# Kernel tuning notes

Hardware: AMD Instinct MI355X
Metric: run time of the kernel (lower is better)

Reference implementation:

```python
import jax, jax.numpy as jnp
import numpy as np

DIM = 256
NUM_HEADS = 8
RATIO = 4
K_SAMPLES = 2
B, C, H, W = 2, 256, 64, 64


def setup_inputs() -> dict:
    key = jax.random.key(0)
    ks = jax.random.split(key, 12)
    N_low = (H // RATIO) * (W // RATIO)
    s = 0.02
    return {
        "q_high_feat": jax.random.normal(ks[0], (B, C, H, W), dtype=jnp.float32),
        "k_high_feat": jax.random.normal(ks[1], (B, C, H, W), dtype=jnp.float32),
        "v_high_feat": jax.random.normal(ks[2], (B, C, H, W), dtype=jnp.float32),
        "coarse_attn_map": jax.random.uniform(ks[3], (B, N_low, N_low), dtype=jnp.float32),
        "Wq": jax.random.normal(ks[4], (C, C), dtype=jnp.float32) * s,
        "bq": jnp.zeros((C,), dtype=jnp.float32),
        "Wk": jax.random.normal(ks[5], (C, C), dtype=jnp.float32) * s,
        "bk": jnp.zeros((C,), dtype=jnp.float32),
        "Wv": jax.random.normal(ks[6], (C, C), dtype=jnp.float32) * s,
        "bv": jnp.zeros((C,), dtype=jnp.float32),
        "Wo": jax.random.normal(ks[7], (C, C), dtype=jnp.float32) * s,
        "bo": jnp.zeros((C,), dtype=jnp.float32),
    }


def _sparse_indices(coarse_attn_map, H, W):
    # top-k coarse blocks per low-res query, expanded to high-res key indices
    H_low, W_low = H // RATIO, W // RATIO
    Bm, N_low, _ = coarse_attn_map.shape
    _, topk = jax.lax.top_k(coarse_attn_map, K_SAMPLES)          # (B, N_low, k)
    r0 = (topk // W_low) * RATIO                                  # top-left row
    c0 = (topk % W_low) * RATIO                                   # top-left col
    dr, dc = jnp.meshgrid(jnp.arange(RATIO), jnp.arange(RATIO), indexing='ij')
    dr, dc = dr.reshape(-1), dc.reshape(-1)                       # (ratio^2,)
    rows = r0[..., None] + dr                                     # (B, N_low, k, r2)
    cols = c0[..., None] + dc
    idx1d = (rows * W + cols).reshape(Bm, N_low, -1)              # (B, N_low, k*r2)
    # each low-res query row is repeated ratio^2 times (as in the torch code)
    return jnp.repeat(idx1d, RATIO * RATIO, axis=1)               # (B, N_high, K)


def reference(q_high_feat, k_high_feat, v_high_feat, coarse_attn_map,
              Wq, bq, Wk, bk, Wv, bv, Wo, bo):
    Bm, Cm, Hm, Wm = q_high_feat.shape
    N = Hm * Wm
    hd = Cm // NUM_HEADS
    scale = hd ** -0.5

    q_seq = q_high_feat.reshape(Bm, Cm, N).transpose(0, 2, 1)     # (B, N, C)
    k_seq = k_high_feat.reshape(Bm, Cm, N).transpose(0, 2, 1)
    v_seq = v_high_feat.reshape(Bm, Cm, N).transpose(0, 2, 1)

    final_idx = _sparse_indices(coarse_attn_map, Hm, Wm)          # (B, N, K)
    K_len = final_idx.shape[-1]

    q_proj = q_seq @ Wq + bq
    k_proj = k_seq @ Wk + bk
    v_proj = v_seq @ Wv + bv

    gather = jax.vmap(lambda p, i: p[i])                          # per-batch gather
    k_sp = gather(k_proj, final_idx)                              # (B, N, K, C)
    v_sp = gather(v_proj, final_idx)

    q = q_proj.reshape(Bm, N, NUM_HEADS, hd).transpose(0, 2, 1, 3)            # (B,h,N,d)
    k = k_sp.reshape(Bm, N, K_len, NUM_HEADS, hd).transpose(0, 3, 1, 2, 4)    # (B,h,N,K,d)
    v = v_sp.reshape(Bm, N, K_len, NUM_HEADS, hd).transpose(0, 3, 1, 2, 4)

    attn = jnp.einsum('bhnd,bhnkd->bhnk', q, k) * scale
    attn = jax.nn.softmax(attn, axis=-1)
    x = jnp.einsum('bhnk,bhnkd->bhnd', attn, v)
    x = x.transpose(0, 2, 1, 3).reshape(Bm, N, Cm)
    out = x @ Wo + bo
    return out.transpose(0, 2, 1).reshape(Bm, Cm, Hm, Wm)
```

## Files before the change

kernel.cpp:

```cpp
#include <hip/hip_runtime.h>
#include <hip/hip_bf16.h>
#include <cstddef>

#define BB 2
#define CC 256
#define HH 64
#define WW 64
#define NN 4096
#define NH 8
#define HD 32
#define NLOW 256
#define KLEN 32

typedef __attribute__((ext_vector_type(8))) short short8;
typedef __attribute__((ext_vector_type(4))) float float4v;

__device__ __forceinline__ float b2f(short s) {
    union { unsigned u; float f; } x;
    x.u = ((unsigned)(unsigned short)s) << 16;
    return x.f;
}
__device__ __forceinline__ short f2b(float f) {
    __hip_bfloat16 h = __float2bfloat16(f);
    return __builtin_bit_cast(short, h);
}

__global__ __launch_bounds__(256) void topk_kernel(const float* __restrict__ coarse,
                                                   int* __restrict__ fidx) {
    const int w = threadIdx.x >> 6, l = threadIdx.x & 63;
    const int row = blockIdx.x * 4 + w;
    const float* r = coarse + (size_t)row * NLOW;
    float4v x = *(const float4v*)&r[l * 4];
    const int base = l * 4;
    float v1 = x[0]; int i1 = base;
    float v2 = x[1]; int i2 = base + 1;
    if (v2 > v1) { float tv = v1; v1 = v2; v2 = tv; int ti = i1; i1 = i2; i2 = ti; }
    #pragma unroll
    for (int j = 2; j < 4; ++j) {
        float e = x[j]; int ei = base + j;
        if (e > v1)      { v2 = v1; i2 = i1; v1 = e; i1 = ei; }
        else if (e > v2) { v2 = e;  i2 = ei; }
    }
    #pragma unroll
    for (int off = 1; off < 64; off <<= 1) {
        float ov1 = __shfl_xor(v1, off), ov2 = __shfl_xor(v2, off);
        int   oi1 = __shfl_xor(i1, off), oi2 = __shfl_xor(i2, off);
        bool aw = (v1 > ov1) || (v1 == ov1 && i1 < oi1);
        float nv1 = aw ? v1 : ov1;  int ni1 = aw ? i1 : oi1;
        float c1v = aw ? ov1 : v1;  int c1i = aw ? oi1 : i1;
        float c2v = aw ? v2 : ov2;  int c2i = aw ? i2 : oi2;
        bool bw = (c1v > c2v) || (c1v == c2v && c1i < c2i);
        v1 = nv1; i1 = ni1;
        v2 = bw ? c1v : c2v; i2 = bw ? c1i : c2i;
    }
    if (l < 32) {
        int s = l >> 4, jj = l & 15;
        int idx = s ? i2 : i1;
        int rr = jj >> 2, cc2 = jj & 3;
        fidx[(size_t)row * KLEN + l] =
            ((idx >> 4) * 4 + rr) * WW + (idx & 15) * 4 + cc2;
    }
}

__device__ __forceinline__ void trans_tile(const float* __restrict__ src, size_t soff,
                                           int sld, short* __restrict__ dst,
                                           size_t doff, int dld) {
    __shared__ float tile[64 * 65];
    const int t = threadIdx.x;
    #pragma unroll
    for (int p = 0; p < 4; ++p) {
        int r  = p * 16 + (t >> 4);
        int c4 = (t & 15) * 4;
        float4v v = *(const float4v*)&src[soff + (size_t)r * sld + c4];
        tile[r * 65 + c4 + 0] = v[0];
        tile[r * 65 + c4 + 1] = v[1];
        tile[r * 65 + c4 + 2] = v[2];
        tile[r * 65 + c4 + 3] = v[3];
    }
    __syncthreads();
    #pragma unroll
    for (int p = 0; p < 2; ++p) {
        int n  = p * 32 + (t >> 3);
        int c0 = (t & 7) * 8;
        short8 o;
        #pragma unroll
        for (int j = 0; j < 8; ++j) o[j] = f2b(tile[(c0 + j) * 65 + n]);
        *(short8*)&dst[doff + (size_t)n * dld + c0] = o;
    }
}

__global__ __launch_bounds__(256) void transpose_feat(
    const float* __restrict__ q, const float* __restrict__ k,
    const float* __restrict__ v, short* __restrict__ qt,
    short* __restrict__ kt, short* __restrict__ vt) {
    const int z = blockIdx.z;
    const float* src = (z < 2) ? q : (z < 4) ? k : v;
    short* dst       = (z < 2) ? qt : (z < 4) ? kt : vt;
    const int b = z & 1;
    const int n0 = blockIdx.x * 64, c0 = blockIdx.y * 64;
    trans_tile(src, (size_t)b * CC * NN + (size_t)c0 * NN + n0, NN,
               dst, ((size_t)b * NN + n0) * CC + c0, CC);
}

__global__ __launch_bounds__(256) void transpose_w(
    const float* __restrict__ Wq, const float* __restrict__ Wk,
    const float* __restrict__ Wv, const float* __restrict__ Wo,
    short* __restrict__ Wt) {
    const int z = blockIdx.z;
    const float* src = (z == 0) ? Wq : (z == 1) ? Wk : (z == 2) ? Wv : Wo;
    short* dst = Wt + (size_t)z * CC * CC;
    const int co0 = blockIdx.x * 64, ci0 = blockIdx.y * 64;
    trans_tile(src, (size_t)ci0 * CC + co0, CC,
               dst, (size_t)co0 * CC + ci0, CC);
}

__device__ __forceinline__ void gemm_core_64x64(
    const short* __restrict__ A, int am0, const short* __restrict__ Bt, int bn0,
    short* As, short* Bs, float4v acc[4]) {
    const int t = threadIdx.x;
    const int w = t >> 6, lane = t & 63;
    const int l16 = lane & 15, quad = lane >> 4;
    for (int k0 = 0; k0 < CC; k0 += 64) {
        __syncthreads();
        #pragma unroll
        for (int g = 0; g < 2; ++g) {
            int p = (w * 2 + g) * 64 + lane;
            int m = p >> 3;
            int cl8 = (((p & 7) ^ (m & 7)) << 3);
            short8 av = *(const short8*)(A  + (size_t)(am0 + m) * CC + k0 + cl8);
            short8 bv = *(const short8*)(Bt + (size_t)(bn0 + m) * CC + k0 + cl8);
            *(short8*)((char*)As + (size_t)p * 16) = av;
            *(short8*)((char*)Bs + (size_t)p * 16) = bv;
        }
        __syncthreads();
        #pragma unroll
        for (int s = 0; s < 2; ++s) {
            const int Ra = 16 * w + l16;
            short8 af = *(const short8*)((const char*)As + Ra * 128 +
                                         (((s * 4 + quad) ^ (Ra & 7)) << 4));
            #pragma unroll
            for (int nt = 0; nt < 4; ++nt) {
                const int Rb = nt * 16 + l16;
                short8 bf = *(const short8*)((const char*)Bs + Rb * 128 +
                                             (((s * 4 + quad) ^ (Rb & 7)) << 4));
                acc[nt] = __builtin_amdgcn_mfma_f32_16x16x32_bf16(af, bf, acc[nt], 0, 0, 0);
            }
        }
    }
}

__global__ __launch_bounds__(256) void proj_gemm(
    const short* __restrict__ qt, const short* __restrict__ kt,
    const short* __restrict__ vt, const short* __restrict__ Wt,
    const float* __restrict__ bq, const float* __restrict__ bk,
    const float* __restrict__ bv,
    short* __restrict__ qp, short* __restrict__ kp, short* __restrict__ vp) {
    const int which = blockIdx.z;
    const short* A  = which == 0 ? qt : which == 1 ? kt : vt;
    const short* B  = Wt + (size_t)which * CC * CC;
    const float* bias = which == 0 ? bq : which == 1 ? bk : bv;
    short* outp     = which == 0 ? qp : which == 1 ? kp : vp;
    const int am0 = blockIdx.x * 64;
    const int nt0 = blockIdx.y * 64;

    __shared__ short As[64 * 64];
    __shared__ short Bs[64 * 64];
    float4v acc[4];
    #pragma unroll
    for (int i = 0; i < 4; ++i) acc[i] = (float4v)(0.f);

    gemm_core_64x64(A, am0, B, nt0, As, Bs, acc);

    const int t = threadIdx.x;
    const int w = t >> 6, lane = t & 63;
    const int l16 = lane & 15, quad = lane >> 4;
    #pragma unroll
    for (int nt = 0; nt < 4; ++nt) {
        int col = nt0 + nt * 16 + l16;
        float bv_ = bias[col];
        #pragma unroll
        for (int r = 0; r < 4; ++r) {
            int m = am0 + 16 * w + quad * 4 + r;
            outp[(size_t)m * CC + col] = f2b(acc[nt][r] + bv_);
        }
    }
}

#define KSTR 264

__global__ __launch_bounds__(256) void attn_kernel(
    const short* __restrict__ qp, const short* __restrict__ kp,
    const short* __restrict__ vp, const int* __restrict__ fidx,
    short* __restrict__ xo) {
    const int low = blockIdx.x, b = blockIdx.y;
    const int t = threadIdx.x;

    __shared__ short Ks[32 * KSTR];
    __shared__ short Vs[32 * KSTR];
    __shared__ int idx_s[KLEN];

    if (t < KLEN) {
        int idx = fidx[(size_t)(b * NLOW + low) * KLEN + t];
        idx_s[t] = idx < 0 ? 0 : (idx > NN - 1 ? NN - 1 : idx);
    }
    __syncthreads();

    const int* kpi = (const int*)kp;
    const int* vpi = (const int*)vp;
    const int half = t >> 7, col = t & 127;
    for (int j = 0; j < KLEN; j += 2) {
        int key = j + half;
        size_t base = (size_t)(b * NN + idx_s[key]) * (CC / 2);
        ((int*)&Ks[key * KSTR])[col] = kpi[base + col];
        ((int*)&Vs[key * KSTR])[col] = vpi[base + col];
    }
    __syncthreads();

    const int qi = t >> 4, h = (t >> 1) & 7, dh = t & 1;
    const int n = low * 16 + qi;
    const short* qrow = qp + (size_t)(b * NN + n) * CC + h * HD;

    float qv[HD];
    #pragma unroll
    for (int c = 0; c < 4; ++c) {
        short8 v = *(const short8*)&qrow[c * 8];
        #pragma unroll
        for (int e = 0; e < 8; ++e) qv[c * 8 + e] = b2f(v[e]);
    }

    const float scale = 0.17677669529663687f;
    float sc[KLEN];
    float mx = -1e30f;
    for (int j = 0; j < KLEN; ++j) {
        const short* kr = &Ks[j * KSTR + h * HD];
        float s = 0.f;
        #pragma unroll
        for (int c = 0; c < 4; ++c) {
            short8 v = *(const short8*)&kr[c * 8];
            #pragma unroll
            for (int e = 0; e < 8; ++e) s += qv[c * 8 + e] * b2f(v[e]);
        }
        s *= scale;
        sc[j] = s;
        mx = fmaxf(mx, s);
    }
    float denom = 0.f;
    #pragma unroll
    for (int j = 0; j < KLEN; ++j) { sc[j] = __expf(sc[j] - mx); denom += sc[j]; }
    const float inv = 1.f / denom;

    float ov[16];
    #pragma unroll
    for (int d = 0; d < 16; ++d) ov[d] = 0.f;
    for (int j = 0; j < KLEN; ++j) {
        float p = sc[j] * inv;
        const short* vr = &Vs[j * KSTR + h * HD + dh * 16];
        #pragma unroll
        for (int c = 0; c < 2; ++c) {
            short8 v = *(const short8*)&vr[c * 8];
            #pragma unroll
            for (int e = 0; e < 8; ++e) ov[c * 8 + e] += p * b2f(v[e]);
        }
    }

    short* xrow = xo + (size_t)(b * NN + n) * CC + h * HD + dh * 16;
    #pragma unroll
    for (int c = 0; c < 2; ++c) {
        short8 v;
        #pragma unroll
        for (int e = 0; e < 8; ++e) v[e] = f2b(ov[c * 8 + e]);
        *(short8*)&xrow[c * 8] = v;
    }
}

__global__ __launch_bounds__(256) void outproj_gemm(
    const short* __restrict__ x, const short* __restrict__ Wto,
    const float* __restrict__ bo, float* __restrict__ out) {
    const int mt  = blockIdx.x;
    const int am0 = mt * 64;
    const int nt0 = blockIdx.y * 64;
    const int b   = mt >> 6;
    const int n0  = (mt & 63) * 64;

    __shared__ short As[64 * 64];
    __shared__ short Bs[64 * 64];
    __shared__ float Cs[64 * 65];

    float4v acc[4];
    #pragma unroll
    for (int i = 0; i < 4; ++i) acc[i] = (float4v)(0.f);

    gemm_core_64x64(x, am0, Wto, nt0, As, Bs, acc);

    const int t = threadIdx.x;
    const int w = t >> 6, lane = t & 63;
    const int l16 = lane & 15, quad = lane >> 4;
    __syncthreads();
    #pragma unroll
    for (int nt = 0; nt < 4; ++nt) {
        float bias = bo[nt0 + nt * 16 + l16];
        #pragma unroll
        for (int r = 0; r < 4; ++r) {
            int m = 16 * w + quad * 4 + r;
            Cs[m * 65 + nt * 16 + l16] = acc[nt][r] + bias;
        }
    }
    __syncthreads();
    #pragma unroll
    for (int p = 0; p < 16; ++p) {
        int cl = (t >> 6) + 4 * p;
        int nl = t & 63;
        out[(size_t)(b * CC + nt0 + cl) * NN + n0 + nl] = Cs[nl * 65 + cl];
    }
}

extern "C" void kernel_launch(void* const* d_in, const int* in_sizes, int n_in,
                              void* d_out, int out_size, void* d_ws, size_t ws_size,
                              hipStream_t stream) {
    const float* q      = (const float*)d_in[0];
    const float* k      = (const float*)d_in[1];
    const float* v      = (const float*)d_in[2];
    const float* coarse = (const float*)d_in[3];
    const float* Wq     = (const float*)d_in[4];
    const float* bq     = (const float*)d_in[5];
    const float* Wk     = (const float*)d_in[6];
    const float* bk     = (const float*)d_in[7];
    const float* Wv     = (const float*)d_in[8];
    const float* bv     = (const float*)d_in[9];
    const float* Wo     = (const float*)d_in[10];
    const float* bo     = (const float*)d_in[11];

    char* ws = (char*)d_ws;
    const size_t MB4 = (size_t)BB * NN * CC * 2;
    short* qt = (short*)(ws);
    short* kt = (short*)(ws + MB4);
    short* vt = (short*)(ws + 2 * MB4);
    short* qp = (short*)(ws + 3 * MB4);
    short* kp = (short*)(ws + 4 * MB4);
    short* vp = (short*)(ws + 5 * MB4);
    short* Wt = (short*)(ws + 6 * MB4);
    int* fidx = (int*)(ws + 6 * MB4 + 4 * (size_t)CC * CC * 2);
    short* xo = qt;

    topk_kernel<<<128, 256, 0, stream>>>(coarse, fidx);
    transpose_feat<<<dim3(64, 4, 6), 256, 0, stream>>>(q, k, v, qt, kt, vt);
    transpose_w<<<dim3(4, 4, 4), 256, 0, stream>>>(Wq, Wk, Wv, Wo, Wt);
    proj_gemm<<<dim3(128, 4, 3), 256, 0, stream>>>(qt, kt, vt, Wt, bq, bk, bv,
                                                   qp, kp, vp);
    attn_kernel<<<dim3(NLOW, BB), 256, 0, stream>>>(qp, kp, vp, fidx, xo);
    outproj_gemm<<<dim3(128, 4), 256, 0, stream>>>(xo, Wt + 3 * CC * CC, bo,
                                                   (float*)d_out);
}
```

Baseline: 129.9 us.

## Merge prep kernels, enlarge projection GEMM M-tile, split attention dot across lane pair

Folds topk, feature transpose and weight transpose into one prep_kernel launch, removing two kernel launches. The projection GEMM now computes 128-row tiles per block so each loaded B fragment is reused across two M sub-tiles, halving the grid. The attention kernel has each thread of a pair load only half of q and k and combine partial dot products with a shuffle, which cuts register use and duplicated loads. The cost is more registers per GEMM thread and fewer blocks in the projection grid.

```diff
diff --git a/kernel.cpp b/kernel.cpp
--- a/kernel.cpp
+++ b/kernel.cpp
@@ -25,10 +25,63 @@
     return __builtin_bit_cast(short, h);
 }
 
-__global__ __launch_bounds__(256) void topk_kernel(const float* __restrict__ coarse,
-                                                   int* __restrict__ fidx) {
+__device__ __forceinline__ void trans_tile(const float* __restrict__ src, size_t soff,
+                                           int sld, short* __restrict__ dst,
+                                           size_t doff, int dld) {
+    __shared__ float tile[64 * 65];
+    const int t = threadIdx.x;
+    #pragma unroll
+    for (int p = 0; p < 4; ++p) {
+        int r  = p * 16 + (t >> 4);
+        int c4 = (t & 15) * 4;
+        float4v v = *(const float4v*)&src[soff + (size_t)r * sld + c4];
+        tile[r * 65 + c4 + 0] = v[0];
+        tile[r * 65 + c4 + 1] = v[1];
+        tile[r * 65 + c4 + 2] = v[2];
+        tile[r * 65 + c4 + 3] = v[3];
+    }
+    __syncthreads();
+    #pragma unroll
+    for (int p = 0; p < 2; ++p) {
+        int n  = p * 32 + (t >> 3);
+        int c0 = (t & 7) * 8;
+        short8 o;
+        #pragma unroll
+        for (int j = 0; j < 8; ++j) o[j] = f2b(tile[(c0 + j) * 65 + n]);
+        *(short8*)&dst[doff + (size_t)n * dld + c0] = o;
+    }
+}
+
+__global__ __launch_bounds__(256) void prep_kernel(
+    const float* __restrict__ q, const float* __restrict__ k,
+    const float* __restrict__ v, const float* __restrict__ Wq,
+    const float* __restrict__ Wk, const float* __restrict__ Wv,
+    const float* __restrict__ Wo, const float* __restrict__ coarse,
+    short* __restrict__ qt, short* __restrict__ kt, short* __restrict__ vt,
+    short* __restrict__ Wt, int* __restrict__ fidx) {
+    const int z = blockIdx.z;
+    if (z < 6) {
+        const float* src = (z < 2) ? q : (z < 4) ? k : v;
+        short* dst       = (z < 2) ? qt : (z < 4) ? kt : vt;
+        const int b = z & 1;
+        const int n0 = blockIdx.x * 64, c0 = blockIdx.y * 64;
+        trans_tile(src, (size_t)b * CC * NN + (size_t)c0 * NN + n0, NN,
+                   dst, ((size_t)b * NN + n0) * CC + c0, CC);
+        return;
+    }
+    const int id = blockIdx.y * 64 + blockIdx.x;
+    if (id < 64) {
+        const int wz = id >> 4, tile = id & 15;
+        const float* src = (wz == 0) ? Wq : (wz == 1) ? Wk : (wz == 2) ? Wv : Wo;
+        short* dst = Wt + (size_t)wz * CC * CC;
+        const int co0 = (tile >> 2) * 64, ci0 = (tile & 3) * 64;
+        trans_tile(src, (size_t)ci0 * CC + co0, CC,
+                   dst, (size_t)co0 * CC + ci0, CC);
+        return;
+    }
+    if (id >= 192) return;
     const int w = threadIdx.x >> 6, l = threadIdx.x & 63;
-    const int row = blockIdx.x * 4 + w;
+    const int row = (id - 64) * 4 + w;
     const float* r = coarse + (size_t)row * NLOW;
     float4v x = *(const float4v*)&r[l * 4];
     const int base = l * 4;
@@ -62,88 +115,50 @@
     }
 }
 
-__device__ __forceinline__ void trans_tile(const float* __restrict__ src, size_t soff,
-                                           int sld, short* __restrict__ dst,
-                                           size_t doff, int dld) {
-    __shared__ float tile[64 * 65];
-    const int t = threadIdx.x;
-    #pragma unroll
-    for (int p = 0; p < 4; ++p) {
-        int r  = p * 16 + (t >> 4);
-        int c4 = (t & 15) * 4;
-        float4v v = *(const float4v*)&src[soff + (size_t)r * sld + c4];
-        tile[r * 65 + c4 + 0] = v[0];
-        tile[r * 65 + c4 + 1] = v[1];
-        tile[r * 65 + c4 + 2] = v[2];
-        tile[r * 65 + c4 + 3] = v[3];
-    }
-    __syncthreads();
-    #pragma unroll
-    for (int p = 0; p < 2; ++p) {
-        int n  = p * 32 + (t >> 3);
-        int c0 = (t & 7) * 8;
-        short8 o;
-        #pragma unroll
-        for (int j = 0; j < 8; ++j) o[j] = f2b(tile[(c0 + j) * 65 + n]);
-        *(short8*)&dst[doff + (size_t)n * dld + c0] = o;
-    }
-}
-
-__global__ __launch_bounds__(256) void transpose_feat(
-    const float* __restrict__ q, const float* __restrict__ k,
-    const float* __restrict__ v, short* __restrict__ qt,
-    short* __restrict__ kt, short* __restrict__ vt) {
-    const int z = blockIdx.z;
-    const float* src = (z < 2) ? q : (z < 4) ? k : v;
-    short* dst       = (z < 2) ? qt : (z < 4) ? kt : vt;
-    const int b = z & 1;
-    const int n0 = blockIdx.x * 64, c0 = blockIdx.y * 64;
-    trans_tile(src, (size_t)b * CC * NN + (size_t)c0 * NN + n0, NN,
-               dst, ((size_t)b * NN + n0) * CC + c0, CC);
-}
-
-__global__ __launch_bounds__(256) void transpose_w(
-    const float* __restrict__ Wq, const float* __restrict__ Wk,
-    const float* __restrict__ Wv, const float* __restrict__ Wo,
-    short* __restrict__ Wt) {
-    const int z = blockIdx.z;
-    const float* src = (z == 0) ? Wq : (z == 1) ? Wk : (z == 2) ? Wv : Wo;
-    short* dst = Wt + (size_t)z * CC * CC;
-    const int co0 = blockIdx.x * 64, ci0 = blockIdx.y * 64;
-    trans_tile(src, (size_t)ci0 * CC + co0, CC,
-               dst, (size_t)co0 * CC + ci0, CC);
-}
-
-__device__ __forceinline__ void gemm_core_64x64(
+template <int MT>
+__device__ __forceinline__ void gemm_core(
     const short* __restrict__ A, int am0, const short* __restrict__ Bt, int bn0,
-    short* As, short* Bs, float4v acc[4]) {
+    short* As, short* Bs, float4v acc[MT][4]) {
     const int t = threadIdx.x;
     const int w = t >> 6, lane = t & 63;
     const int l16 = lane & 15, quad = lane >> 4;
     for (int k0 = 0; k0 < CC; k0 += 64) {
         __syncthreads();
         #pragma unroll
+        for (int g = 0; g < 2 * MT; ++g) {
+            int p = (w * 2 * MT + g) * 64 + lane;
+            int m = p >> 3;
+            int cl8 = (((p & 7) ^ (m & 7)) << 3);
+            *(short8*)((char*)As + (size_t)p * 16) =
+                *(const short8*)(A + (size_t)(am0 + m) * CC + k0 + cl8);
+        }
+        #pragma unroll
         for (int g = 0; g < 2; ++g) {
             int p = (w * 2 + g) * 64 + lane;
             int m = p >> 3;
             int cl8 = (((p & 7) ^ (m & 7)) << 3);
-            short8 av = *(const short8*)(A  + (size_t)(am0 + m) * CC + k0 + cl8);
-            short8 bv = *(const short8*)(Bt + (size_t)(bn0 + m) * CC + k0 + cl8);
-            *(short8*)((char*)As + (size_t)p * 16) = av;
-            *(short8*)((char*)Bs + (size_t)p * 16) = bv;
+            *(short8*)((char*)Bs + (size_t)p * 16) =
+                *(const short8*)(Bt + (size_t)(bn0 + m) * CC + k0 + cl8);
         }
         __syncthreads();
         #pragma unroll
         for (int s = 0; s < 2; ++s) {
-            const int Ra = 16 * w + l16;
-            short8 af = *(const short8*)((const char*)As + Ra * 128 +
-                                         (((s * 4 + quad) ^ (Ra & 7)) << 4));
+            short8 bf[4];
             #pragma unroll
             for (int nt = 0; nt < 4; ++nt) {
                 const int Rb = nt * 16 + l16;
-                short8 bf = *(const short8*)((const char*)Bs + Rb * 128 +
-                                             (((s * 4 + quad) ^ (Rb & 7)) << 4));
-                acc[nt] = __builtin_amdgcn_mfma_f32_16x16x32_bf16(af, bf, acc[nt], 0, 0, 0);
+                bf[nt] = *(const short8*)((const char*)Bs + Rb * 128 +
+                                          (((s * 4 + quad) ^ (Rb & 7)) << 4));
+            }
+            #pragma unroll
+            for (int mt = 0; mt < MT; ++mt) {
+                const int Ra = mt * 64 + 16 * w + l16;
+                short8 af = *(const short8*)((const char*)As + Ra * 128 +
+                                             (((s * 4 + quad) ^ (Ra & 7)) << 4));
+                #pragma unroll
+                for (int nt = 0; nt < 4; ++nt)
+                    acc[mt][nt] = __builtin_amdgcn_mfma_f32_16x16x32_bf16(
+                        af, bf[nt], acc[mt][nt], 0, 0, 0);
             }
         }
     }
@@ -160,30 +175,34 @@
     const short* B  = Wt + (size_t)which * CC * CC;
     const float* bias = which == 0 ? bq : which == 1 ? bk : bv;
     short* outp     = which == 0 ? qp : which == 1 ? kp : vp;
-    const int am0 = blockIdx.x * 64;
+    const int am0 = blockIdx.x * 128;
     const int nt0 = blockIdx.y * 64;
 
-    __shared__ short As[64 * 64];
+    __shared__ short As[128 * 64];
     __shared__ short Bs[64 * 64];
-    float4v acc[4];
-    #pragma unroll
-    for (int i = 0; i < 4; ++i) acc[i] = (float4v)(0.f);
-
-    gemm_core_64x64(A, am0, B, nt0, As, Bs, acc);
+    float4v acc[2][4];
+    #pragma unroll
+    for (int i = 0; i < 2; ++i)
+        #pragma unroll
+        for (int j = 0; j < 4; ++j) acc[i][j] = (float4v)(0.f);
+
+    gemm_core<2>(A, am0, B, nt0, As, Bs, acc);
 
     const int t = threadIdx.x;
     const int w = t >> 6, lane = t & 63;
     const int l16 = lane & 15, quad = lane >> 4;
     #pragma unroll
-    for (int nt = 0; nt < 4; ++nt) {
-        int col = nt0 + nt * 16 + l16;
-        float bv_ = bias[col];
-        #pragma unroll
-        for (int r = 0; r < 4; ++r) {
-            int m = am0 + 16 * w + quad * 4 + r;
-            outp[(size_t)m * CC + col] = f2b(acc[nt][r] + bv_);
-        }
-    }
+    for (int mt = 0; mt < 2; ++mt)
+        #pragma unroll
+        for (int nt = 0; nt < 4; ++nt) {
+            int col = nt0 + nt * 16 + l16;
+            float bv_ = bias[col];
+            #pragma unroll
+            for (int r = 0; r < 4; ++r) {
+                int m = am0 + mt * 64 + 16 * w + quad * 4 + r;
+                outp[(size_t)m * CC + col] = f2b(acc[mt][nt][r] + bv_);
+            }
+        }
 }
 
 #define KSTR 264
@@ -218,11 +237,11 @@
 
     const int qi = t >> 4, h = (t >> 1) & 7, dh = t & 1;
     const int n = low * 16 + qi;
-    const short* qrow = qp + (size_t)(b * NN + n) * CC + h * HD;
-
-    float qv[HD];
-    #pragma unroll
-    for (int c = 0; c < 4; ++c) {
+    const short* qrow = qp + (size_t)(b * NN + n) * CC + h * HD + dh * 16;
+
+    float qv[16];
+    #pragma unroll
+    for (int c = 0; c < 2; ++c) {
         short8 v = *(const short8*)&qrow[c * 8];
         #pragma unroll
         for (int e = 0; e < 8; ++e) qv[c * 8 + e] = b2f(v[e]);
@@ -230,19 +249,22 @@
 
     const float scale = 0.17677669529663687f;
     float sc[KLEN];
+    for (int j = 0; j < KLEN; ++j) {
+        const short* kr = &Ks[j * KSTR + h * HD + dh * 16];
+        float s = 0.f;
+        #pragma unroll
+        for (int c = 0; c < 2; ++c) {
+            short8 v = *(const short8*)&kr[c * 8];
+            #pragma unroll
+            for (int e = 0; e < 8; ++e) s += qv[c * 8 + e] * b2f(v[e]);
+        }
+        sc[j] = s;
+    }
     float mx = -1e30f;
+    #pragma unroll
     for (int j = 0; j < KLEN; ++j) {
-        const short* kr = &Ks[j * KSTR + h * HD];
-        float s = 0.f;
-        #pragma unroll
-        for (int c = 0; c < 4; ++c) {
-            short8 v = *(const short8*)&kr[c * 8];
-            #pragma unroll
-            for (int e = 0; e < 8; ++e) s += qv[c * 8 + e] * b2f(v[e]);
-        }
-        s *= scale;
-        sc[j] = s;
-        mx = fmaxf(mx, s);
+        sc[j] = (sc[j] + __shfl_xor(sc[j], 1)) * scale;
+        mx = fmaxf(mx, sc[j]);
     }
     float denom = 0.f;
     #pragma unroll
@@ -286,11 +308,11 @@
     __shared__ short Bs[64 * 64];
     __shared__ float Cs[64 * 65];
 
-    float4v acc[4];
-    #pragma unroll
-    for (int i = 0; i < 4; ++i) acc[i] = (float4v)(0.f);
-
-    gemm_core_64x64(x, am0, Wto, nt0, As, Bs, acc);
+    float4v acc[1][4];
+    #pragma unroll
+    for (int j = 0; j < 4; ++j) acc[0][j] = (float4v)(0.f);
+
+    gemm_core<1>(x, am0, Wto, nt0, As, Bs, acc);
 
     const int t = threadIdx.x;
     const int w = t >> 6, lane = t & 63;
@@ -302,7 +324,7 @@
         #pragma unroll
         for (int r = 0; r < 4; ++r) {
             int m = 16 * w + quad * 4 + r;
-            Cs[m * 65 + nt * 16 + l16] = acc[nt][r] + bias;
+            Cs[m * 65 + nt * 16 + l16] = acc[0][nt][r] + bias;
         }
     }
     __syncthreads();
@@ -342,11 +364,10 @@
     int* fidx = (int*)(ws + 6 * MB4 + 4 * (size_t)CC * CC * 2);
     short* xo = qt;
 
-    topk_kernel<<<128, 256, 0, stream>>>(coarse, fidx);
-    transpose_feat<<<dim3(64, 4, 6), 256, 0, stream>>>(q, k, v, qt, kt, vt);
-    transpose_w<<<dim3(4, 4, 4), 256, 0, stream>>>(Wq, Wk, Wv, Wo, Wt);
-    proj_gemm<<<dim3(128, 4, 3), 256, 0, stream>>>(qt, kt, vt, Wt, bq, bk, bv,
-                                                   qp, kp, vp);
+    prep_kernel<<<dim3(64, 4, 7), 256, 0, stream>>>(q, k, v, Wq, Wk, Wv, Wo,
+                                                    coarse, qt, kt, vt, Wt, fidx);
+    proj_gemm<<<dim3(64, 4, 3), 256, 0, stream>>>(qt, kt, vt, Wt, bq, bk, bv,
+                                                  qp, kp, vp);
     attn_kernel<<<dim3(NLOW, BB), 256, 0, stream>>>(qp, kp, vp, fidx, xo);
     outproj_gemm<<<dim3(128, 4), 256, 0, stream>>>(xo, Wt + 3 * CC * CC, bo,
                                                    (float*)d_out);
```

Result: faster. 125.1 us (-3.7%).
